# Performance work log

Measured on AMD Instinct MI355X. Metric: run time of the kernel, lower is better.

## Reference

```python
import jax, jax.numpy as jnp
import numpy as np
import math

B, T, D = 2, 2048, 1024
H, DH = 16, 64  # n_heads, d_head
ROPE_THETA = 10000.0


def _rope_cos_sin(seq_len, d_head, dtype):
    # inv_freq over even indices, freqs[i,j] = t_i * inv_freq_j, shape [T, d_head//2]
    inv_freq = 1.0 / (ROPE_THETA ** (jnp.arange(0, d_head, 2, dtype=jnp.float32) / d_head))
    freqs = jnp.arange(seq_len, dtype=jnp.float32)[:, None] * inv_freq[None, :]
    # emb = cat(freqs, freqs); we only ever index cos[..., :d_head//2], so keep the half
    cos = jnp.cos(freqs).astype(dtype)[None, :, None, :]  # [1,T,1,DH/2]
    sin = jnp.sin(freqs).astype(dtype)[None, :, None, :]
    return cos, sin


def _apply_rotation(x, cos, sin):
    # x: [B,T,H,DH]; rotate-half style as in the torch module
    x1, x2 = x[..., : x.shape[-1] // 2], x[..., x.shape[-1] // 2 :]
    return jnp.concatenate([x1 * cos - x2 * sin, x1 * sin + x2 * cos], axis=-1)


def setup_inputs() -> dict:
    key = jax.random.key(0)
    k1, k2, k3 = jax.random.split(key, 3)
    x = jax.random.normal(k1, (B, T, D), dtype=jnp.float32)
    # torch Linear weights stored transposed here as [in, out]; init_std=0.02
    Wqkv = jax.random.normal(k2, (D, 3 * D), dtype=jnp.float32) * 0.02
    Wout = jax.random.normal(k3, (D, D), dtype=jnp.float32) * 0.02
    return {"x": x, "Wqkv": Wqkv, "Wout": Wout}


def reference(x, Wqkv, Wout):
    b, t, d = x.shape
    qkv = x @ Wqkv  # [B,T,3D]
    q, k, v = jnp.split(qkv, 3, axis=-1)
    q = q.reshape(b, t, H, DH)
    k = k.reshape(b, t, H, DH)
    v = v.reshape(b, t, H, DH)

    cos, sin = _rope_cos_sin(t, DH, x.dtype)
    q = _apply_rotation(q, cos, sin)
    k = _apply_rotation(k, cos, sin)

    scale = 1.0 / math.sqrt(DH)
    # scores: [B,H,Tq,Tk]
    scores = jnp.einsum("bqhd,bkhd->bhqk", q, k) * scale
    causal = jnp.triu(jnp.ones((t, t), dtype=bool), k=1)
    scores = jnp.where(causal[None, None, :, :], -jnp.inf, scores)
    attn = jax.nn.softmax(scores, axis=-1)
    # dropout in eval mode -> identity
    out = jnp.einsum("bhqk,bkhd->bqhd", attn, v).reshape(b, t, d)
    return out @ Wout
```

## Files before the change

### kernel.cpp

```cpp
#include <hip/hip_runtime.h>
#include <hip/hip_bf16.h>
#include <stdint.h>
#include <math.h>

#define T_SEQ 2048
#define NHEAD 16
#define NBH   32
#define BTROW 4096

typedef __bf16 bf16_t;
typedef __bf16 bf16x4_t __attribute__((ext_vector_type(4)));
typedef __bf16 bf16x8_t __attribute__((ext_vector_type(8)));
typedef float  f32x4_t  __attribute__((ext_vector_type(4)));

#define QSCALE 0.18033688011112042f

__device__ __forceinline__ f32x4_t mfma16(bf16x8_t a, bf16x8_t b, f32x4_t c) {
  return __builtin_amdgcn_mfma_f32_16x16x32_bf16(a, b, c, 0, 0, 0);
}

__device__ __forceinline__ float fast_exp2(float x) {
#if __has_builtin(__builtin_amdgcn_exp2f)
  return __builtin_amdgcn_exp2f(x);
#else
  return exp2f(x);
#endif
}

__device__ __forceinline__ void gl_lds16(const bf16_t* g, bf16_t* l) {
  __builtin_amdgcn_global_load_lds(
      (const __attribute__((address_space(1))) void*)g,
      (__attribute__((address_space(3))) void*)l, 16, 0, 0);
}

__device__ __forceinline__ int tile_off(int r, int k8) {
  int lr = r >> 1;
  int g = (((r & 1) << 2) | k8) ^ (lr & 7);
  return lr * 64 + g * 8;
}
__device__ __forceinline__ int src_off(int c, int K) {
  int lr = c >> 3;
  int gsrc = (c & 7) ^ (lr & 7);
  int row = (lr << 1) | (gsrc >> 2), kb = gsrc & 3;
  return row * K + kb * 8;
}

__global__ __launch_bounds__(256) void k_cast_bf16(const float* __restrict__ in,
                                                   bf16_t* __restrict__ out, int n) {
  int tid = blockIdx.x * blockDim.x + threadIdx.x;
  int stride = gridDim.x * blockDim.x;
  for (int i = tid * 4; i < n; i += stride * 4) {
    float4 a = *(const float4*)(in + i);
    bf16x4_t r = { (bf16_t)a.x, (bf16_t)a.y, (bf16_t)a.z, (bf16_t)a.w };
    *(bf16x4_t*)(out + i) = r;
  }
}

__global__ __launch_bounds__(256) void k_trans_cast(const float* __restrict__ W,
                                                    bf16_t* __restrict__ WT,
                                                    int K, int N) {
  __shared__ float tile[32][33];
  int n0 = blockIdx.x * 32, k0 = blockIdx.y * 32;
  int tx = threadIdx.x & 31, ty = threadIdx.x >> 5;
#pragma unroll
  for (int j = 0; j < 4; j++)
    tile[ty + j * 8][tx] = W[(size_t)(k0 + ty + j * 8) * N + n0 + tx];
  __syncthreads();
#pragma unroll
  for (int j = 0; j < 4; j++)
    WT[(size_t)(n0 + ty + j * 8) * K + k0 + tx] = (bf16_t)tile[tx][ty + j * 8];
}

__global__ __launch_bounds__(256) void k_rope_table(float* __restrict__ cs,
                                                    float* __restrict__ sn) {
  int i = blockIdx.x * blockDim.x + threadIdx.x;
  if (i >= T_SEQ * 32) return;
  int t = i >> 5, j = i & 31;
  float inv = powf(10000.0f, -(float)(2 * j) / 64.0f);
  float f = (float)t * inv;
  cs[i] = cosf(f);
  sn[i] = sinf(f);
}

__global__ __launch_bounds__(256) void k_gemm_qkv(const bf16_t* __restrict__ A,
                                                  const bf16_t* __restrict__ Bt,
                                                  const float* __restrict__ cs,
                                                  const float* __restrict__ sn,
                                                  bf16_t* __restrict__ Qr,
                                                  bf16_t* __restrict__ Kr,
                                                  bf16_t* __restrict__ Vt) {
  const int K = 1024, NT = 32;
  __shared__ __align__(16) unsigned char smem[49152];
  bf16_t* vtile = (bf16_t*)smem;

  int m0 = blockIdx.y * 128, n0 = blockIdx.x * 128;
  int tid = threadIdx.x;
  int lane = tid & 63, w = tid >> 6;
  int wr = w >> 1, wc = w & 1;
  int l15 = lane & 15, l4 = lane >> 4;

  f32x4_t acc[4][4];
#pragma unroll
  for (int m = 0; m < 4; m++)
#pragma unroll
    for (int n = 0; n < 4; n++) acc[m][n] = (f32x4_t){0.f, 0.f, 0.f, 0.f};

  const bf16_t* Ag = A + (size_t)m0 * K;
  const bf16_t* Bg = Bt + (size_t)n0 * K;
  int soff0 = src_off(tid, K), soff1 = src_off(256 + tid, K);
  int dst0 = w * 512, dst1 = 2048 + w * 512;
  int afo[4], bfo[4];
#pragma unroll
  for (int m = 0; m < 4; m++) afo[m] = tile_off(wr * 64 + m * 16 + l15, l4);
#pragma unroll
  for (int n = 0; n < 4; n++) bfo[n] = tile_off(wc * 64 + n * 16 + l15, l4);

  auto stageg = [&](int bufbyte, int k0) {
    bf16_t* As = (bf16_t*)(smem + bufbyte);
    bf16_t* Bs = (bf16_t*)(smem + 8192 + bufbyte);
    gl_lds16(Ag + soff0 + k0, As + dst0);
    gl_lds16(Bg + soff0 + k0, Bs + dst0);
    gl_lds16(Ag + soff1 + k0, As + dst1);
    gl_lds16(Bg + soff1 + k0, Bs + dst1);
  };

#define QKV_BODY(KT, CB)                                                          \
  {                                                                               \
    if ((KT) + 1 < NT) asm volatile("s_waitcnt vmcnt(4)" ::: "memory");           \
    else               asm volatile("s_waitcnt vmcnt(0)" ::: "memory");           \
    __builtin_amdgcn_s_barrier();                                                 \
    if ((KT) + 2 < NT) stageg((((CB) + 2) % 3) * 16384, ((KT) + 2) * 32);         \
    const bf16_t* As = (const bf16_t*)(smem + (CB) * 16384);                      \
    const bf16_t* Bs = (const bf16_t*)(smem + 8192 + (CB) * 16384);               \
    bf16x8_t af[4], bfr[4];                                                       \
    _Pragma("unroll")                                                             \
    for (int m = 0; m < 4; m++) af[m] = *(const bf16x8_t*)(As + afo[m]);          \
    _Pragma("unroll")                                                             \
    for (int n = 0; n < 4; n++) bfr[n] = *(const bf16x8_t*)(Bs + bfo[n]);         \
    _Pragma("unroll")                                                             \
    for (int m = 0; m < 4; m++)                                                   \
      _Pragma("unroll")                                                           \
      for (int n = 0; n < 4; n++) acc[m][n] = mfma16(af[m], bfr[n], acc[m][n]);   \
  }

  stageg(0, 0);
  stageg(16384, 32);
  for (int kt0 = 0; kt0 < 30; kt0 += 3) {
    QKV_BODY(kt0 + 0, 0)
    QKV_BODY(kt0 + 1, 1)
    QKV_BODY(kt0 + 2, 2)
  }
  QKV_BODY(30, 0)
  QKV_BODY(31, 1)
#undef QKV_BODY
  __syncthreads();

  int region = n0 >> 10;
  if (region < 2) {
    bf16_t* dst = region ? Kr : Qr;
    float qs = region ? 1.0f : QSCALE;
    int h = ((n0 & 1023) + wc * 64) >> 6;
#pragma unroll
    for (int m = 0; m < 4; m++)
#pragma unroll
      for (int r = 0; r < 4; r++) {
        int row = m0 + wr * 64 + m * 16 + l4 * 4 + r;
        int b = row >> 11, t = row & 2047;
        size_t obase = ((size_t)(b * NHEAD + h) * T_SEQ + t) * 64;
#pragma unroll
        for (int n = 0; n < 2; n++) {
          int j = n * 16 + l15;
          float c = cs[t * 32 + j], s = sn[t * 32 + j];
          float x1 = acc[m][n][r], x2 = acc[m][n + 2][r];
          dst[obase + j]      = (bf16_t)((x1 * c - x2 * s) * qs);
          dst[obase + 32 + j] = (bf16_t)((x1 * s + x2 * c) * qs);
        }
      }
  } else {
#pragma unroll
    for (int m = 0; m < 4; m++)
#pragma unroll
      for (int n = 0; n < 4; n++)
#pragma unroll
        for (int r = 0; r < 4; r++)
          vtile[(size_t)(wc * 64 + n * 16 + l15) * 132 + wr * 64 + m * 16 + l4 * 4 + r] =
              (bf16_t)acc[m][n][r];
    __syncthreads();
    int colbase = n0 - 2048;
    int b = m0 >> 11, t0l = m0 & 2047;
#pragma unroll
    for (int p = 0; p < 64; p++) {
      int idx = p * 256 + tid;
      int dl = idx >> 7, tl = idx & 127;
      int col = colbase + dl, h = col >> 6, d = col & 63;
      Vt[((size_t)(b * NHEAD + h) * 64 + d) * T_SEQ + t0l + tl] = vtile[(size_t)dl * 132 + tl];
    }
  }
}

__global__ __launch_bounds__(256) void k_gemm2(const bf16_t* __restrict__ A,
                                               const bf16_t* __restrict__ Bt,
                                               float* __restrict__ C) {
  const int N = 1024, K = 1024, NT = 32;
  __shared__ __align__(16) unsigned char smem[36864];
  int m0 = blockIdx.y * 64, n0 = blockIdx.x * 128;
  int tid = threadIdx.x;
  int lane = tid & 63, w = tid >> 6;
  int l15 = lane & 15, l4 = lane >> 4;

  f32x4_t acc[4][2];
#pragma unroll
  for (int m = 0; m < 4; m++)
#pragma unroll
    for (int n = 0; n < 2; n++) acc[m][n] = (f32x4_t){0.f, 0.f, 0.f, 0.f};

  const bf16_t* Ag = A + (size_t)m0 * K;
  const bf16_t* Bg = Bt + (size_t)n0 * K;
  int soff0 = src_off(tid, K), soff1 = src_off(256 + tid, K);
  int dstA = w * 512, dstB0 = w * 512, dstB1 = 2048 + w * 512;
  int afo[4], bfo[2];
#pragma unroll
  for (int m = 0; m < 4; m++) afo[m] = tile_off(m * 16 + l15, l4);
#pragma unroll
  for (int n = 0; n < 2; n++) bfo[n] = tile_off(w * 32 + n * 16 + l15, l4);

  auto stageg = [&](int bufbyte, int k0) {
    bf16_t* As = (bf16_t*)(smem + bufbyte);
    bf16_t* Bs = (bf16_t*)(smem + 4096 + bufbyte);
    gl_lds16(Ag + soff0 + k0, As + dstA);
    gl_lds16(Bg + soff0 + k0, Bs + dstB0);
    gl_lds16(Bg + soff1 + k0, Bs + dstB1);
  };

#define G2_BODY(KT, CB)                                                           \
  {                                                                               \
    if ((KT) + 1 < NT) asm volatile("s_waitcnt vmcnt(3)" ::: "memory");           \
    else               asm volatile("s_waitcnt vmcnt(0)" ::: "memory");           \
    __builtin_amdgcn_s_barrier();                                                 \
    if ((KT) + 2 < NT) stageg((((CB) + 2) % 3) * 12288, ((KT) + 2) * 32);         \
    const bf16_t* As = (const bf16_t*)(smem + (CB) * 12288);                      \
    const bf16_t* Bs = (const bf16_t*)(smem + 4096 + (CB) * 12288);               \
    bf16x8_t af[4], bfr[2];                                                       \
    _Pragma("unroll")                                                             \
    for (int m = 0; m < 4; m++) af[m] = *(const bf16x8_t*)(As + afo[m]);          \
    _Pragma("unroll")                                                             \
    for (int n = 0; n < 2; n++) bfr[n] = *(const bf16x8_t*)(Bs + bfo[n]);         \
    _Pragma("unroll")                                                             \
    for (int m = 0; m < 4; m++)                                                   \
      _Pragma("unroll")                                                           \
      for (int n = 0; n < 2; n++) acc[m][n] = mfma16(af[m], bfr[n], acc[m][n]);   \
  }

  stageg(0, 0);
  stageg(12288, 32);
  for (int kt0 = 0; kt0 < 30; kt0 += 3) {
    G2_BODY(kt0 + 0, 0)
    G2_BODY(kt0 + 1, 1)
    G2_BODY(kt0 + 2, 2)
  }
  G2_BODY(30, 0)
  G2_BODY(31, 1)
#undef G2_BODY

#pragma unroll
  for (int m = 0; m < 4; m++)
#pragma unroll
    for (int n = 0; n < 2; n++)
#pragma unroll
      for (int r = 0; r < 4; r++) {
        int row = m0 + m * 16 + l4 * 4 + r;
        int col = n0 + w * 32 + n * 16 + l15;
        C[(size_t)row * N + col] = acc[m][n][r];
      }
}

__global__ __launch_bounds__(512, 4) void k_attn(const bf16_t* __restrict__ Qr,
                                                 const bf16_t* __restrict__ Kr,
                                                 const bf16_t* __restrict__ Vt,
                                                 bf16_t* __restrict__ Ob) {
  __shared__ __align__(16) bf16_t Ks[2][2][64 * 64];
  __shared__ __align__(16) bf16_t Vs[2][2][64 * 64];
  __shared__ __align__(16) bf16_t Ps[8][16 * 64];
  int flat = blockIdx.x;
  int swz = (flat & 7) * 64 + (flat >> 3);
  int pair = swz & 15, bh = swz >> 4;
  int b = bh >> 4, h = bh & 15;
  int tid = threadIdx.x, lane = tid & 63, w = tid >> 6;
  int grp = w >> 2, wl = w & 3;
  int l15 = lane & 15, l4 = lane >> 4;

  const bf16_t* Kbh = Kr + (size_t)bh * T_SEQ * 64;
  const bf16_t* Vbh = Vt + (size_t)bh * 64 * T_SEQ;

  int srow = tid >> 3;
  int sk8 = (tid & 7) ^ (srow & 7);

  auto stage = [&](int buf, int i) {
#pragma unroll
    for (int tp = 0; tp < 2; tp++) {
      int kb = (2 * i + tp) * 64;
      gl_lds16(Kbh + (size_t)(kb + srow) * 64 + sk8 * 8, &Ks[buf][tp][0] + (size_t)w * 512);
      gl_lds16(Vbh + (size_t)srow * T_SEQ + kb + sk8 * 8, &Vs[buf][tp][0] + (size_t)w * 512);
    }
  };

  char* myPs = (char*)&Ps[w][0];

  bf16x8_t ones;
#pragma unroll
  for (int i = 0; i < 8; i++) ones[i] = (bf16_t)1.0f;

  for (int pass = 0; pass < 2; pass++) {
    int qb = pass ? (31 - pair) : pair;
    int q0 = qb * 64;
    int niter = (qb + 2) >> 1;

    bf16x8_t qf[2];
    size_t qbase = ((size_t)bh * T_SEQ + q0 + wl * 16 + l15) * 64;
    qf[0] = *(const bf16x8_t*)(Qr + qbase + l4 * 8);
    qf[1] = *(const bf16x8_t*)(Qr + qbase + 32 + l4 * 8);

    f32x4_t o[4];
#pragma unroll
    for (int n = 0; n < 4; n++) o[n] = (f32x4_t){0.f, 0.f, 0.f, 0.f};
    f32x4_t ls = (f32x4_t){0.f, 0.f, 0.f, 0.f};
    float m_s = -1e30f;

    stage(0, 0);

    for (int i = 0; i < niter; i++) {
      int cur = i & 1;
      asm volatile("s_waitcnt vmcnt(0)" ::: "memory");
      __builtin_amdgcn_s_barrier();
      if (i + 1 < niter) stage(cur ^ 1, i + 1);

      int t = 2 * i + grp;
      if (t <= qb) {
        const bf16_t* Kt = &Ks[cur][grp][0];
        const bf16_t* Vtl = &Vs[cur][grp][0];

        f32x4_t s[4];
        __builtin_amdgcn_s_setprio(1);
#pragma unroll
        for (int n = 0; n < 4; n++) {
          int rowK = n * 16 + l15;
          const bf16_t* kp = Kt + (size_t)rowK * 64;
          int sw = rowK & 7;
          bf16x8_t kf0 = *(const bf16x8_t*)(kp + (l4 ^ sw) * 8);
          bf16x8_t kf1 = *(const bf16x8_t*)(kp + ((l4 ^ 4) ^ sw) * 8);
          s[n] = (f32x4_t){0.f, 0.f, 0.f, 0.f};
          s[n] = mfma16(kf0, qf[0], s[n]);
          s[n] = mfma16(kf1, qf[1], s[n]);
        }
        __builtin_amdgcn_s_setprio(0);

        bf16x8_t vfr[8];
#pragma unroll
        for (int ks = 0; ks < 2; ks++)
#pragma unroll
          for (int n = 0; n < 4; n++) {
            int rowV = n * 16 + l15;
            vfr[ks * 4 + n] = *(const bf16x8_t*)(Vtl + (size_t)rowV * 64 +
                                                 (((ks * 4 + l4) ^ (rowV & 7)) * 8));
          }

        if (t == qb) {
#pragma unroll
          for (int n = 0; n < 4; n++)
#pragma unroll
            for (int r = 0; r < 4; r++)
              if (n * 16 + l4 * 4 + r > wl * 16 + l15) s[n][r] = -1e30f;
        }

        float t0 = fmaxf(fmaxf(s[0][0], s[0][1]), fmaxf(s[0][2], s[0][3]));
        float t1 = fmaxf(fmaxf(s[1][0], s[1][1]), fmaxf(s[1][2], s[1][3]));
        float t2 = fmaxf(fmaxf(s[2][0], s[2][1]), fmaxf(s[2][2], s[2][3]));
        float t3 = fmaxf(fmaxf(s[3][0], s[3][1]), fmaxf(s[3][2], s[3][3]));
        float mloc = fmaxf(fmaxf(t0, t1), fmaxf(t2, t3));

        if (__any(mloc - m_s > 8.0f)) {
          float mx = fmaxf(mloc, __shfl_xor(mloc, 16, 64));
          mx = fmaxf(mx, __shfl_xor(mx, 32, 64));
          float mnew = fmaxf(m_s, mx);
          float alpha = fast_exp2(m_s - mnew);
          m_s = mnew;
          float ar[4];
#pragma unroll
          for (int r = 0; r < 4; r++) ar[r] = __shfl(alpha, l4 * 4 + r, 64);
#pragma unroll
          for (int n = 0; n < 4; n++)
#pragma unroll
            for (int r = 0; r < 4; r++) o[n][r] *= ar[r];
#pragma unroll
          for (int r = 0; r < 4; r++) ls[r] *= ar[r];
        }

#pragma unroll
        for (int n = 0; n < 4; n++) {
#pragma unroll
          for (int r = 0; r < 4; r++) s[n][r] = fast_exp2(s[n][r] - m_s);
          bf16x4_t pk = { (bf16_t)s[n][0], (bf16_t)s[n][1], (bf16_t)s[n][2], (bf16_t)s[n][3] };
          *(bf16x4_t*)(myPs + l15 * 128 +
                       ((((n << 1) | (l4 >> 1)) ^ (l15 & 7)) << 4) + ((l4 & 1) << 3)) = pk;
        }

        __builtin_amdgcn_s_setprio(1);
#pragma unroll
        for (int ks = 0; ks < 2; ks++) {
          bf16x8_t pa = *(const bf16x8_t*)(myPs + l15 * 128 +
                                           ((((ks << 2) | l4) ^ (l15 & 7)) << 4));
          ls = mfma16(pa, ones, ls);
#pragma unroll
          for (int n = 0; n < 4; n++) o[n] = mfma16(pa, vfr[ks * 4 + n], o[n]);
        }
        __builtin_amdgcn_s_setprio(0);
      }
    }

    __syncthreads();
    float* mg = (float*)&Ks[0][0][0];
    int base = (wl * 64 + lane) * 25;
    if (grp == 1) {
#pragma unroll
      for (int n = 0; n < 4; n++)
#pragma unroll
        for (int r = 0; r < 4; r++) mg[base + n * 4 + r] = o[n][r];
#pragma unroll
      for (int r = 0; r < 4; r++) mg[base + 16 + r] = ls[r];
#pragma unroll
      for (int r = 0; r < 4; r++) mg[base + 20 + r] = __shfl(m_s, l4 * 4 + r, 64);
    }
    __syncthreads();
    if (grp == 0) {
#pragma unroll
      for (int r = 0; r < 4; r++) {
        float mA = __shfl(m_s, l4 * 4 + r, 64);
        float mB = mg[base + 20 + r];
        float mF = fmaxf(mA, mB);
        float fA = fast_exp2(mA - mF), fB = fast_exp2(mB - mF);
        float lF = ls[r] * fA + mg[base + 16 + r] * fB;
        float ir = 1.0f / lF;
        int q = q0 + wl * 16 + l4 * 4 + r;
        size_t off = ((size_t)(b * T_SEQ + q)) * 1024 + h * 64;
#pragma unroll
        for (int n = 0; n < 4; n++) {
          float val = o[n][r] * fA + mg[base + n * 4 + r] * fB;
          Ob[off + n * 16 + l15] = (bf16_t)(val * ir);
        }
      }
    }
    __syncthreads();
  }
}

extern "C" void kernel_launch(void* const* d_in, const int* in_sizes, int n_in,
                              void* d_out, int out_size, void* d_ws, size_t ws_size,
                              hipStream_t stream) {
  const float* x    = (const float*)d_in[0];
  const float* Wqkv = (const float*)d_in[1];
  const float* Wout = (const float*)d_in[2];
  float* out = (float*)d_out;
  char* ws = (char*)d_ws;

  bf16_t* wqkvT = (bf16_t*)(ws + 0);
  bf16_t* woutT = (bf16_t*)(ws + 6291456);
  bf16_t* xb    = (bf16_t*)(ws + 8388608);
  bf16_t* Qr    = (bf16_t*)(ws + 41943040);
  bf16_t* Kr    = (bf16_t*)(ws + 50331648);
  bf16_t* Vt    = (bf16_t*)(ws + 58720256);
  float*  cs    = (float*)(ws + 67108864);
  float*  sn    = (float*)(ws + 67371008);
  bf16_t* Ob    = xb;

  k_cast_bf16<<<2048, 256, 0, stream>>>(x, xb, 4096 * 1024);
  k_trans_cast<<<dim3(3072 / 32, 1024 / 32), 256, 0, stream>>>(Wqkv, wqkvT, 1024, 3072);
  k_trans_cast<<<dim3(1024 / 32, 1024 / 32), 256, 0, stream>>>(Wout, woutT, 1024, 1024);
  k_rope_table<<<(T_SEQ * 32) / 256, 256, 0, stream>>>(cs, sn);

  k_gemm_qkv<<<dim3(3072 / 128, 4096 / 128), 256, 0, stream>>>(xb, wqkvT, cs, sn, Qr, Kr, Vt);
  k_attn<<<512, 512, 0, stream>>>(Qr, Kr, Vt, Ob);
  k_gemm2<<<dim3(1024 / 128, 4096 / 64), 256, 0, stream>>>(Ob, woutT, out);
}
```

Measured before the change: 104.1 us.

## Merge prep kernels into one launch and single-buffer K tiles in attention

Four preprocessing kernels (x cast, two weight transpose-casts, RoPE table) become one block-indexed launch, which removes three launch gaps and the serialization between them. In the attention kernel the K tile is now single-buffered. The next K/V prefetch is issued only after every wave has finished its QK^T MFMAs, guarded by a mid-iteration barrier, and the wait-and-barrier moves to the end of each iteration. This frees LDS, which may allow more occupancy, but adds a barrier per iteration and shortens the window in which loads overlap compute.

```diff
diff --git a/kernel.cpp b/kernel.cpp
--- a/kernel.cpp
+++ b/kernel.cpp
@@ -45,23 +45,11 @@
   return row * K + kb * 8;
 }
 
-__global__ __launch_bounds__(256) void k_cast_bf16(const float* __restrict__ in,
-                                                   bf16_t* __restrict__ out, int n) {
-  int tid = blockIdx.x * blockDim.x + threadIdx.x;
-  int stride = gridDim.x * blockDim.x;
-  for (int i = tid * 4; i < n; i += stride * 4) {
-    float4 a = *(const float4*)(in + i);
-    bf16x4_t r = { (bf16_t)a.x, (bf16_t)a.y, (bf16_t)a.z, (bf16_t)a.w };
-    *(bf16x4_t*)(out + i) = r;
-  }
-}
-
-__global__ __launch_bounds__(256) void k_trans_cast(const float* __restrict__ W,
-                                                    bf16_t* __restrict__ WT,
-                                                    int K, int N) {
-  __shared__ float tile[32][33];
-  int n0 = blockIdx.x * 32, k0 = blockIdx.y * 32;
-  int tx = threadIdx.x & 31, ty = threadIdx.x >> 5;
+__device__ __forceinline__ void trans_tile(const float* __restrict__ W,
+                                           bf16_t* __restrict__ WT,
+                                           int K, int N, int n0, int k0,
+                                           float (*tile)[33], int tid) {
+  int tx = tid & 31, ty = tid >> 5;
 #pragma unroll
   for (int j = 0; j < 4; j++)
     tile[ty + j * 8][tx] = W[(size_t)(k0 + ty + j * 8) * N + n0 + tx];
@@ -71,15 +59,37 @@
     WT[(size_t)(n0 + ty + j * 8) * K + k0 + tx] = (bf16_t)tile[tx][ty + j * 8];
 }
 
-__global__ __launch_bounds__(256) void k_rope_table(float* __restrict__ cs,
-                                                    float* __restrict__ sn) {
-  int i = blockIdx.x * blockDim.x + threadIdx.x;
-  if (i >= T_SEQ * 32) return;
-  int t = i >> 5, j = i & 31;
-  float inv = powf(10000.0f, -(float)(2 * j) / 64.0f);
-  float f = (float)t * inv;
-  cs[i] = cosf(f);
-  sn[i] = sinf(f);
+__global__ __launch_bounds__(256) void k_prep(const float* __restrict__ x,
+                                              const float* __restrict__ Wqkv,
+                                              const float* __restrict__ Wout,
+                                              bf16_t* __restrict__ xb,
+                                              bf16_t* __restrict__ wqkvT,
+                                              bf16_t* __restrict__ woutT,
+                                              float* __restrict__ cs,
+                                              float* __restrict__ sn) {
+  __shared__ float tile[32][33];
+  int blk = blockIdx.x, tid = threadIdx.x;
+  if (blk < 2048) {
+    const int n = 4096 * 1024, stride = 2048 * 256;
+    for (int i = (blk * 256 + tid) * 4; i < n; i += stride * 4) {
+      float4 a = *(const float4*)(x + i);
+      bf16x4_t r = { (bf16_t)a.x, (bf16_t)a.y, (bf16_t)a.z, (bf16_t)a.w };
+      *(bf16x4_t*)(xb + i) = r;
+    }
+  } else if (blk < 5120) {
+    int bb = blk - 2048;
+    trans_tile(Wqkv, wqkvT, 1024, 3072, (bb % 96) * 32, (bb / 96) * 32, tile, tid);
+  } else if (blk < 6144) {
+    int bb = blk - 5120;
+    trans_tile(Wout, woutT, 1024, 1024, (bb % 32) * 32, (bb / 32) * 32, tile, tid);
+  } else {
+    int i = (blk - 6144) * 256 + tid;
+    int t = i >> 5, j = i & 31;
+    float inv = powf(10000.0f, -(float)(2 * j) / 64.0f);
+    float f = (float)t * inv;
+    cs[i] = cosf(f);
+    sn[i] = sinf(f);
+  }
 }
 
 __global__ __launch_bounds__(256) void k_gemm_qkv(const bf16_t* __restrict__ A,
@@ -278,7 +288,7 @@
                                                  const bf16_t* __restrict__ Kr,
                                                  const bf16_t* __restrict__ Vt,
                                                  bf16_t* __restrict__ Ob) {
-  __shared__ __align__(16) bf16_t Ks[2][2][64 * 64];
+  __shared__ __align__(16) bf16_t Ks[2][64 * 64];
   __shared__ __align__(16) bf16_t Vs[2][2][64 * 64];
   __shared__ __align__(16) bf16_t Ps[8][16 * 64];
   int flat = blockIdx.x;
@@ -295,11 +305,17 @@
   int srow = tid >> 3;
   int sk8 = (tid & 7) ^ (srow & 7);
 
-  auto stage = [&](int buf, int i) {
+  auto stageK = [&](int i) {
 #pragma unroll
     for (int tp = 0; tp < 2; tp++) {
       int kb = (2 * i + tp) * 64;
-      gl_lds16(Kbh + (size_t)(kb + srow) * 64 + sk8 * 8, &Ks[buf][tp][0] + (size_t)w * 512);
+      gl_lds16(Kbh + (size_t)(kb + srow) * 64 + sk8 * 8, &Ks[tp][0] + (size_t)w * 512);
+    }
+  };
+  auto stageV = [&](int buf, int i) {
+#pragma unroll
+    for (int tp = 0; tp < 2; tp++) {
+      int kb = (2 * i + tp) * 64;
       gl_lds16(Vbh + (size_t)srow * T_SEQ + kb + sk8 * 8, &Vs[buf][tp][0] + (size_t)w * 512);
     }
   };
@@ -326,20 +342,19 @@
     f32x4_t ls = (f32x4_t){0.f, 0.f, 0.f, 0.f};
     float m_s = -1e30f;
 
-    stage(0, 0);
+    stageK(0);
+    stageV(0, 0);
+    asm volatile("s_waitcnt vmcnt(0)" ::: "memory");
+    __builtin_amdgcn_s_barrier();
 
     for (int i = 0; i < niter; i++) {
       int cur = i & 1;
-      asm volatile("s_waitcnt vmcnt(0)" ::: "memory");
-      __builtin_amdgcn_s_barrier();
-      if (i + 1 < niter) stage(cur ^ 1, i + 1);
-
       int t = 2 * i + grp;
-      if (t <= qb) {
-        const bf16_t* Kt = &Ks[cur][grp][0];
-        const bf16_t* Vtl = &Vs[cur][grp][0];
-
-        f32x4_t s[4];
+      bool act = (t <= qb);
+
+      f32x4_t s[4];
+      if (act) {
+        const bf16_t* Kt = &Ks[grp][0];
         __builtin_amdgcn_s_setprio(1);
 #pragma unroll
         for (int n = 0; n < 4; n++) {
@@ -353,7 +368,16 @@
           s[n] = mfma16(kf1, qf[1], s[n]);
         }
         __builtin_amdgcn_s_setprio(0);
-
+      }
+      __builtin_amdgcn_s_barrier();
+
+      if (i + 1 < niter) {
+        stageK(i + 1);
+        stageV(cur ^ 1, i + 1);
+      }
+
+      if (act) {
+        const bf16_t* Vtl = &Vs[cur][grp][0];
         bf16x8_t vfr[8];
 #pragma unroll
         for (int ks = 0; ks < 2; ks++)
@@ -415,10 +439,13 @@
         }
         __builtin_amdgcn_s_setprio(0);
       }
+
+      asm volatile("s_waitcnt vmcnt(0)" ::: "memory");
+      __builtin_amdgcn_s_barrier();
     }
 
     __syncthreads();
-    float* mg = (float*)&Ks[0][0][0];
+    float* mg = (float*)&Vs[0][0][0];
     int base = (wl * 64 + lane) * 25;
     if (grp == 1) {
 #pragma unroll
@@ -472,11 +499,7 @@
   float*  sn    = (float*)(ws + 67371008);
   bf16_t* Ob    = xb;
 
-  k_cast_bf16<<<2048, 256, 0, stream>>>(x, xb, 4096 * 1024);
-  k_trans_cast<<<dim3(3072 / 32, 1024 / 32), 256, 0, stream>>>(Wqkv, wqkvT, 1024, 3072);
-  k_trans_cast<<<dim3(1024 / 32, 1024 / 32), 256, 0, stream>>>(Wout, woutT, 1024, 1024);
-  k_rope_table<<<(T_SEQ * 32) / 256, 256, 0, stream>>>(cs, sn);
-
+  k_prep<<<6400, 256, 0, stream>>>(x, Wqkv, Wout, xb, wqkvT, woutT, cs, sn);
   k_gemm_qkv<<<dim3(3072 / 128, 4096 / 128), 256, 0, stream>>>(xb, wqkvT, cs, sn, Qr, Kr, Vt);
   k_attn<<<512, 512, 0, stream>>>(Qr, Kr, Vt, Ob);
   k_gemm2<<<dim3(1024 / 128, 4096 / 64), 256, 0, stream>>>(Ob, woutT, out);
```

Result: faster. 99.25 us (-4.6%).
